# Performance work log

Measured on AMD Instinct MI355X. Metric: run time of the kernel, lower is better.

Reference implementation:

```python
import jax, jax.numpy as jnp
import numpy as np
import math

B, L, H, D, HID = 2, 1024, 16, 64, 1024  # batch, seq, heads, head_dim, hidden_size


def _rope_tables(seq_len, dim):
    inv_freq = 1.0 / (10000.0 ** (jnp.arange(0, dim, 2, dtype=jnp.float32) / dim))
    t = jnp.arange(seq_len, dtype=jnp.float32)
    freqs = jnp.outer(t, inv_freq)            # (L, D/2)
    emb = jnp.concatenate([freqs, freqs], -1)  # (L, D)
    return jnp.cos(emb), jnp.sin(emb)


def _rotate_half(x):
    x1, x2 = jnp.split(x, 2, axis=-1)
    return jnp.concatenate([-x2, x1], axis=-1)


def _apply_rope(x, cos, sin):
    # x: (B,H,L,D); cos/sin: (1,1,L,D)
    return x * cos + _rotate_half(x) * sin


def setup_inputs() -> dict:
    key = jax.random.key(0)
    ks = jax.random.split(key, 8)
    s = 0.02
    return {
        "x": jax.random.normal(ks[0], (B, L, HID), jnp.float32),
        "w_qkv": jax.random.normal(ks[1], (HID, 3 * H * D), jnp.float32) * s,
        "w_o": jax.random.normal(ks[2], (H * D, HID), jnp.float32) * s,
        "log_p": jax.random.normal(ks[3], (H, 1, 1), jnp.float32) * 0.02,
        "log_a": jax.random.normal(ks[4], (H, 1, 1), jnp.float32) * 0.02,
        "w1": jax.random.normal(ks[5], (2 * H, 2 * H), jnp.float32) * s,
        "b1": jnp.zeros((2 * H,), jnp.float32),
        "w2": jax.random.normal(ks[6], (2 * H, H), jnp.float32) * s,
        "b2": jnp.zeros((H,), jnp.float32),
    }


def _forward(x, w_qkv, w_o, log_p, log_a, w1, b1, w2, b2):
    Bx, Lx, _ = x.shape
    qkv = jnp.dot(x, w_qkv).reshape(Bx, Lx, 3, H, D)
    qkv = jnp.transpose(qkv, (2, 0, 3, 1, 4))  # (3,B,H,L,D)
    q, k, v = qkv[0], qkv[1], qkv[2]

    cos, sin = _rope_tables(Lx, D)
    cos, sin = cos[None, None], sin[None, None]
    q = _apply_rope(q, cos, sin)
    k = _apply_rope(k, cos, sin)

    scale = 1.0 / math.sqrt(D)
    scores = jnp.einsum('bhid,bhjd->bhij', q, k) * scale  # (B,H,L,L)

    # Kerple bias: -p * log1p(a * |m-n|), per head
    pos = jnp.arange(Lx, dtype=jnp.float32)
    dist = jnp.abs(pos[None, :] - pos[:, None])            # (L,L)
    p = jax.nn.softplus(log_p)
    a = jax.nn.softplus(log_a)
    kerple = -p * jnp.log1p(a * dist[None])                # (H,L,L)

    # DAPE MLP refinement over head channel
    attn_t = jnp.transpose(scores, (0, 2, 3, 1))           # (B,L,L,H)
    kerple_t = jnp.broadcast_to(jnp.transpose(kerple, (1, 2, 0))[None], attn_t.shape)
    combined = jnp.concatenate([attn_t, kerple_t], axis=-1)  # (B,L,L,2H)
    hdn = jax.nn.gelu(jnp.dot(combined, w1) + b1, approximate=False)
    refined = jnp.dot(hdn, w2) + b2                        # (B,L,L,H)
    refined = jnp.transpose(refined, (0, 3, 1, 2))         # (B,H,L,L)

    scores = scores + kerple[None] + refined

    causal = jnp.tril(jnp.ones((Lx, Lx), dtype=bool))
    scores = jnp.where(causal[None, None], scores, -jnp.inf)
    weights = jax.nn.softmax(scores, axis=-1)
    out = jnp.einsum('bhij,bhjd->bhid', weights, v)        # (B,H,L,D)
    out = jnp.transpose(out, (0, 2, 1, 3)).reshape(Bx, Lx, H * D)
    return jnp.dot(out, w_o)


def reference(x, w_qkv, w_o, log_p, log_a, w1, b1, w2, b2):
    return _forward(x, w_qkv, w_o, log_p, log_a, w1, b1, w2, b2)
```

## Files before the change

### kernel.cpp

```cpp
#include <hip/hip_runtime.h>
#include <math.h>

#define Bv 2
#define Lv 1024
#define Hv 16
#define Dv 64
#define HIDv 1024

typedef unsigned short u16;
typedef short bf16x8 __attribute__((ext_vector_type(8)));
typedef unsigned short u16x4 __attribute__((ext_vector_type(4)));
typedef float f32x4 __attribute__((ext_vector_type(4)));

__device__ __forceinline__ u16 f2b(float f) {
    union { float f; unsigned u; } v; v.f = f;
    return (u16)((v.u + 0x8000u) >> 16);
}
__device__ __forceinline__ float b2f(u16 h) {
    union { unsigned u; float f; } v; v.u = ((unsigned)h) << 16;
    return v.f;
}

__device__ __forceinline__ void gl2lds16(const u16* g, u16* l) {
    __builtin_amdgcn_global_load_lds(
        (const __attribute__((address_space(1))) unsigned int*)g,
        (__attribute__((address_space(3))) unsigned int*)l,
        16, 0, 0);
}

__device__ __forceinline__ float gelu_fast(float x) {
    float x2 = x * x;
    float inner = __builtin_fmaf(0.044715f * x2, x, x);
    float e = __expf(-1.5957691216057308f * inner);
    return x * __builtin_amdgcn_rcpf(1.0f + e);
}

__global__ __launch_bounds__(256) void qkv_rope(
    const u16* __restrict__ A, const u16* __restrict__ B,
    const float* __restrict__ ctab, const float* __restrict__ stab,
    u16* __restrict__ q, u16* __restrict__ k, u16* __restrict__ vT)
{
    __shared__ __align__(16) char pool[64 * 136 * 2];
    u16* As = (u16*)pool;
    u16* Bs = (u16*)(pool + 8192);
    u16* Ct = (u16*)pool;

    const int m0 = blockIdx.y * 64;
    const int n0 = blockIdx.x * 128;
    const int K = 1024;

    const int tid = threadIdx.x;
    const int lane = tid & 63;
    const int wave = tid >> 6;
    const int wm0 = (wave >> 1) * 32;
    const int wn0 = (wave & 1) * 64;
    const int fr = lane & 15;
    const int fq = lane >> 4;

    f32x4 acc[2][4];
    #pragma unroll
    for (int i = 0; i < 2; ++i)
        #pragma unroll
        for (int j = 0; j < 4; ++j) acc[i][j] = (f32x4){0.f, 0.f, 0.f, 0.f};

    for (int k0 = 0; k0 < K; k0 += 32) {
        {
            int r = tid >> 2, ch = tid & 3;
            gl2lds16(A + (long long)(m0 + r) * K + k0 + ch * 8, &As[tid * 8]);
        }
        #pragma unroll
        for (int it = 0; it < 2; ++it) {
            int cid = tid + it * 256;
            int r = cid >> 2, ch = cid & 3;
            gl2lds16(B + (long long)(n0 + r) * K + k0 + ch * 8, &Bs[cid * 8]);
        }
        __syncthreads();
        bf16x8 af[2], bfr[4];
        #pragma unroll
        for (int i = 0; i < 2; ++i)
            af[i] = *(const bf16x8*)&As[(wm0 + i * 16 + fr) * 32 + fq * 8];
        #pragma unroll
        for (int j = 0; j < 4; ++j)
            bfr[j] = *(const bf16x8*)&Bs[(wn0 + j * 16 + fr) * 32 + fq * 8];
        #pragma unroll
        for (int i = 0; i < 2; ++i)
            #pragma unroll
            for (int j = 0; j < 4; ++j)
                acc[i][j] = __builtin_amdgcn_mfma_f32_16x16x32_bf16(
                    af[i], bfr[j], acc[i][j], 0, 0, 0);
        __syncthreads();
    }

    const int b = m0 >> 10;

    if (n0 >= 2048) {
        #pragma unroll
        for (int i = 0; i < 2; ++i)
            #pragma unroll
            for (int j = 0; j < 4; ++j) {
                int vcol = (n0 - 2048) + wn0 + j * 16 + fr;
                int head = vcol >> 6, d = vcol & 63;
                int l = ((m0 + wm0 + i * 16 + fq * 4) & 1023);
                u16 o[4];
                #pragma unroll
                for (int r = 0; r < 4; ++r) o[r] = f2b(acc[i][j][r]);
                *(u16x4*)&vT[((long long)(b * 16 + head) * 64 + d) * 1024 + l] =
                    *(u16x4*)o;
            }
        return;
    }

    #pragma unroll
    for (int i = 0; i < 2; ++i)
        #pragma unroll
        for (int j = 0; j < 4; ++j)
            #pragma unroll
            for (int r = 0; r < 4; ++r)
                Ct[(wm0 + i * 16 + fq * 4 + r) * 136 + wn0 + j * 16 + fr] =
                    f2b(acc[i][j][r]);
    __syncthreads();

    u16* dst = (n0 >= 1024) ? k : q;
    const int nh = n0 & 1023;
    #pragma unroll
    for (int c = 0; c < 4; ++c) {
        int cid = tid + c * 256;
        int row = cid >> 4, kc = cid & 15;
        int l = (m0 + row) & 1023;
        int head = (nh >> 6) + (kc >> 3);
        int d0 = (kc & 7) * 8;
        bf16x8 x  = *(const bf16x8*)&Ct[row * 136 + kc * 8];
        bf16x8 xp = *(const bf16x8*)&Ct[row * 136 + (kc ^ 4) * 8];
        float4 c0 = *(const float4*)&ctab[l * 64 + d0];
        float4 c1 = *(const float4*)&ctab[l * 64 + d0 + 4];
        float4 s0 = *(const float4*)&stab[l * 64 + d0];
        float4 s1 = *(const float4*)&stab[l * 64 + d0 + 4];
        float ct[8] = {c0.x, c0.y, c0.z, c0.w, c1.x, c1.y, c1.z, c1.w};
        float st[8] = {s0.x, s0.y, s0.z, s0.w, s1.x, s1.y, s1.z, s1.w};
        u16 o[8];
        #pragma unroll
        for (int e = 0; e < 8; ++e)
            o[e] = f2b(b2f((u16)x[e]) * ct[e] + b2f((u16)xp[e]) * st[e]);
        *(bf16x8*)&dst[((long long)(b * 16 + head) * 1024 + l) * 64 + d0] =
            *(bf16x8*)o;
    }
}

template<int BM, int BN, int WM, int WN, bool CBF16>
__global__ __launch_bounds__(256) void gemm_bt(
    const u16* __restrict__ A, const u16* __restrict__ B, void* __restrict__ Cv,
    int M, int N, int K, float alpha)
{
    constexpr int NW = BN / WN;
    constexpr int MI = WM / 16;
    constexpr int NI = WN / 16;
    constexpr int LDB = BN + 8;
    constexpr int LDF = BN + 4;
    __shared__ u16 As[BM * 32];
    __shared__ u16 Bs[BN * 32];
    __shared__ u16 Ctb[CBF16 ? BM * LDB : 1];
    __shared__ float Ctf[CBF16 ? 1 : BM * LDF];

    const int m0 = blockIdx.y * BM;
    const int n0 = blockIdx.x * BN;

    const int tid = threadIdx.x;
    const int lane = tid & 63;
    const int wave = tid >> 6;
    const int wm0 = (wave / NW) * WM;
    const int wn0 = (wave % NW) * WN;
    const int fr = lane & 15;
    const int fq = lane >> 4;

    f32x4 acc[MI][NI];
    #pragma unroll
    for (int i = 0; i < MI; ++i)
        #pragma unroll
        for (int j = 0; j < NI; ++j) acc[i][j] = (f32x4){0.f, 0.f, 0.f, 0.f};

    for (int k0 = 0; k0 < K; k0 += 32) {
        #pragma unroll
        for (int it = 0; it < BM / 64; ++it) {
            int cid = tid + it * 256;
            int r = cid >> 2, ch = cid & 3;
            gl2lds16(A + (long long)(m0 + r) * K + k0 + ch * 8, &As[cid * 8]);
        }
        #pragma unroll
        for (int it = 0; it < BN / 64; ++it) {
            int cid = tid + it * 256;
            int r = cid >> 2, ch = cid & 3;
            gl2lds16(B + (long long)(n0 + r) * K + k0 + ch * 8, &Bs[cid * 8]);
        }
        __syncthreads();
        bf16x8 af[MI], bfr[NI];
        #pragma unroll
        for (int i = 0; i < MI; ++i)
            af[i] = *(const bf16x8*)&As[(wm0 + i * 16 + fr) * 32 + fq * 8];
        #pragma unroll
        for (int j = 0; j < NI; ++j)
            bfr[j] = *(const bf16x8*)&Bs[(wn0 + j * 16 + fr) * 32 + fq * 8];
        #pragma unroll
        for (int i = 0; i < MI; ++i)
            #pragma unroll
            for (int j = 0; j < NI; ++j)
                acc[i][j] = __builtin_amdgcn_mfma_f32_16x16x32_bf16(
                    af[i], bfr[j], acc[i][j], 0, 0, 0);
        __syncthreads();
    }

    #pragma unroll
    for (int i = 0; i < MI; ++i)
        #pragma unroll
        for (int j = 0; j < NI; ++j)
            #pragma unroll
            for (int r = 0; r < 4; ++r) {
                int row = wm0 + i * 16 + fq * 4 + r;
                int col = wn0 + j * 16 + fr;
                float v = acc[i][j][r] * alpha;
                if (CBF16) Ctb[row * LDB + col] = f2b(v);
                else       Ctf[row * LDF + col] = v;
            }
    __syncthreads();
    if (CBF16) {
        constexpr int CPR = BN / 8;
        #pragma unroll
        for (int c = 0; c < (BM * BN) / (8 * 256); ++c) {
            int cid = tid + c * 256;
            int row = cid / CPR, kc = cid % CPR;
            *(bf16x8*)((u16*)Cv + (long long)(m0 + row) * N + n0 + kc * 8) =
                *(const bf16x8*)&Ctb[row * LDB + kc * 8];
        }
    } else {
        constexpr int CPR = BN / 4;
        #pragma unroll
        for (int c = 0; c < (BM * BN) / (4 * 256); ++c) {
            int cid = tid + c * 256;
            int row = cid / CPR, kc = cid % CPR;
            *(float4*)((float*)Cv + (long long)(m0 + row) * N + n0 + kc * 4) =
                *(const float4*)&Ctf[row * LDF + kc * 4];
        }
    }
}

__global__ __launch_bounds__(256) void qk_direct(
    const u16* __restrict__ Q, const u16* __restrict__ K, u16* __restrict__ S)
{
    const int m0 = blockIdx.y * 128;
    const int n0 = blockIdx.x * 128;
    if (n0 > m0) return;
    const u16* A = Q + (long long)blockIdx.z * 65536;
    const u16* B = K + (long long)blockIdx.z * 65536;
    u16* C = S + (long long)blockIdx.z * 1048576;

    __shared__ u16 Ct[128 * 136];

    const int tid = threadIdx.x;
    const int lane = tid & 63;
    const int wave = tid >> 6;
    const int wm0 = (wave >> 1) * 64;
    const int wn0 = (wave & 1) * 64;
    const int fr = lane & 15;
    const int fq = lane >> 4;

    bf16x8 af[4][2], bfr[4][2];
    #pragma unroll
    for (int i = 0; i < 4; ++i)
        #pragma unroll
        for (int p = 0; p < 2; ++p) {
            af[i][p]  = *(const bf16x8*)&A[(m0 + wm0 + i * 16 + fr) * 64 + p * 32 + fq * 8];
            bfr[i][p] = *(const bf16x8*)&B[(n0 + wn0 + i * 16 + fr) * 64 + p * 32 + fq * 8];
        }

    f32x4 acc[4][4];
    #pragma unroll
    for (int i = 0; i < 4; ++i)
        #pragma unroll
        for (int j = 0; j < 4; ++j) acc[i][j] = (f32x4){0.f, 0.f, 0.f, 0.f};

    #pragma unroll
    for (int p = 0; p < 2; ++p)
        #pragma unroll
        for (int i = 0; i < 4; ++i)
            #pragma unroll
            for (int j = 0; j < 4; ++j)
                acc[i][j] = __builtin_amdgcn_mfma_f32_16x16x32_bf16(
                    af[i][p], bfr[j][p], acc[i][j], 0, 0, 0);

    #pragma unroll
    for (int i = 0; i < 4; ++i)
        #pragma unroll
        for (int j = 0; j < 4; ++j)
            #pragma unroll
            for (int r = 0; r < 4; ++r)
                Ct[(wm0 + i * 16 + fq * 4 + r) * 136 + wn0 + j * 16 + fr] =
                    f2b(acc[i][j][r] * 0.125f);
    __syncthreads();
    #pragma unroll
    for (int c = 0; c < 8; ++c) {
        int cid = tid + c * 256;
        int row = cid >> 4, kc = cid & 15;
        *(bf16x8*)&C[(long long)(m0 + row) * 1024 + n0 + kc * 8] =
            *(const bf16x8*)&Ct[row * 136 + kc * 8];
    }
}

__global__ __launch_bounds__(256) void pv_direct(
    const u16* __restrict__ W, const u16* __restrict__ VT, u16* __restrict__ O)
{
    const int m0 = blockIdx.x * 64;
    const int bh = blockIdx.y;
    const u16* A = W + (long long)bh * 1048576;
    const u16* B = VT + (long long)bh * 65536;
    const int b = bh >> 4, h = bh & 15;

    __shared__ u16 Ct[64 * 72];

    const int tid = threadIdx.x;
    const int lane = tid & 63;
    const int wave = tid >> 6;
    const int wm0 = (wave >> 1) * 32;
    const int wn0 = (wave & 1) * 32;
    const int fr = lane & 15;
    const int fq = lane >> 4;

    f32x4 acc[2][2];
    #pragma unroll
    for (int i = 0; i < 2; ++i)
        #pragma unroll
        for (int j = 0; j < 2; ++j) acc[i][j] = (f32x4){0.f, 0.f, 0.f, 0.f};

    const int Kend = m0 + 64;
    for (int k0 = 0; k0 < Kend; k0 += 64) {
        bf16x8 af[2][2], bfr[2][2];
        #pragma unroll
        for (int p = 0; p < 2; ++p) {
            #pragma unroll
            for (int i = 0; i < 2; ++i)
                af[p][i] = *(const bf16x8*)&A[(m0 + wm0 + i * 16 + fr) * 1024 + k0 + p * 32 + fq * 8];
            #pragma unroll
            for (int j = 0; j < 2; ++j)
                bfr[p][j] = *(const bf16x8*)&B[(wn0 + j * 16 + fr) * 1024 + k0 + p * 32 + fq * 8];
        }
        #pragma unroll
        for (int p = 0; p < 2; ++p)
            #pragma unroll
            for (int i = 0; i < 2; ++i)
                #pragma unroll
                for (int j = 0; j < 2; ++j)
                    acc[i][j] = __builtin_amdgcn_mfma_f32_16x16x32_bf16(
                        af[p][i], bfr[p][j], acc[i][j], 0, 0, 0);
    }

    #pragma unroll
    for (int i = 0; i < 2; ++i)
        #pragma unroll
        for (int j = 0; j < 2; ++j)
            #pragma unroll
            for (int r = 0; r < 4; ++r)
                Ct[(wm0 + i * 16 + fq * 4 + r) * 72 + wn0 + j * 16 + fr] =
                    f2b(acc[i][j][r]);
    __syncthreads();
    const long long ob = (long long)b * 1048576 + h * 64;
    #pragma unroll
    for (int c = 0; c < 2; ++c) {
        int cid = tid + c * 256;
        int row = cid >> 3, kc = cid & 7;
        *(bf16x8*)&O[ob + (long long)(m0 + row) * 1024 + kc * 8] =
            *(const bf16x8*)&Ct[row * 72 + kc * 8];
    }
}

__global__ __launch_bounds__(256) void prep(
    const float* __restrict__ x, u16* __restrict__ x_bf,
    const float* __restrict__ w_qkv, u16* __restrict__ wqkvT,
    const float* __restrict__ w_o, u16* __restrict__ woT,
    const float* __restrict__ log_p, const float* __restrict__ log_a,
    u16* __restrict__ ktab, float* __restrict__ ctab, float* __restrict__ stab)
{
    __shared__ float tile[64][65];
    const int bid = blockIdx.x;
    const int tid = threadIdx.x;

    if (bid < 8192) {
        int i = bid * 256 + tid;
        x_bf[i] = f2b(x[i]);
        return;
    }
    if (bid >= 9280) {
        int idx = (bid - 9280) * 256 + tid;
        int e = idx & 65535;
        int l = e >> 6, d = e & 63;
        float inv_freq = __expf((float)(d & 31) * -0.28782313662425574f);
        float arg = (float)l * inv_freq;
        if (idx < 65536) ctab[e] = __cosf(arg);
        else             stab[e] = (d < 32) ? -__sinf(arg) : __sinf(arg);
        return;
    }
    if (bid >= 9216) {
        int idx = (bid - 9216) * 256 + tid;
        int h = idx & 15, dist = idx >> 4;
        float pp = log1pf(__expf(log_p[h]));
        float aa = log1pf(__expf(log_a[h]));
        ktab[idx] = f2b(-pp * log1pf(aa * (float)dist));
        return;
    }
    const float* src; u16* dst; int M, N, bx, by;
    if (bid < 8960) { int t = bid - 8192; bx = t % 48; by = t / 48; src = w_qkv; dst = wqkvT; M = 1024; N = 3072; }
    else            { int t = bid - 8960; bx = t % 16; by = t / 16; src = w_o;   dst = woT;   M = 1024; N = 1024; }
    const int m0 = by * 64, n0 = bx * 64;
    #pragma unroll
    for (int c = 0; c < 4; ++c) {
        int f = tid + c * 256;
        int r = f >> 4, cs = (f & 15) * 4;
        float4 v = *(const float4*)&src[(long long)(m0 + r) * N + n0 + cs];
        tile[r][cs] = v.x; tile[r][cs + 1] = v.y;
        tile[r][cs + 2] = v.z; tile[r][cs + 3] = v.w;
    }
    __syncthreads();
    int nl = tid >> 2, ms = (tid & 3) * 16;
    u16 outv[16];
    #pragma unroll
    for (int c = 0; c < 16; ++c) outv[c] = f2b(tile[ms + c][nl]);
    *(bf16x8*)&dst[(long long)(n0 + nl) * M + m0 + ms]     = *(bf16x8*)&outv[0];
    *(bf16x8*)&dst[(long long)(n0 + nl) * M + m0 + ms + 8] = *(bf16x8*)&outv[8];
}

#define LSTR 1044

__global__ __launch_bounds__(512) void dape_soft(
    u16* __restrict__ S, const u16* __restrict__ ktab,
    const float* __restrict__ w1, const float* __restrict__ b1,
    const float* __restrict__ w2, const float* __restrict__ b2)
{
    const int i = 1023 - blockIdx.x;
    const int b = blockIdx.y;

    __shared__ u16 logits[16 * LSTR];
    __shared__ u16 comb[256 * 36];

    const int tid = threadIdx.x;
    const int lane = tid & 63;
    const int wave = tid >> 6;
    const int fr = lane & 15;
    const int fq = lane >> 4;

    bf16x8 B1a, B1b, B2f, Bid;
    #pragma unroll
    for (int e = 0; e < 8; ++e) {
        int c = fq * 8 + e;
        B1a[e] = (short)f2b(w1[c * 32 + fr]);
        B1b[e] = (short)f2b(w1[c * 32 + 16 + fr]);
        B2f[e] = (short)f2b(w2[c * 16 + fr]);
        Bid[e] = (short)((c == fr || c == 16 + fr) ? 0x3F80 : 0);
    }
    const float b1a = b1[fr], b1b = b1[16 + fr], b2v = b2[fr];

    const long long sbase = (long long)b * 16 * 1048576 + (long long)i * 1024;
    const int nchunk = (i >> 8) + 1;
    const int slast = i >> 8;

    for (int c = 0; c < nchunk; ++c) {
        {
            const int jo = tid & 255;
            const int half = tid >> 8;
            const int j = c * 256 + jo;
            u16 row[8];
            #pragma unroll
            for (int h = 0; h < 8; ++h)
                row[h] = S[sbase + (long long)(half * 8 + h) * 1048576 + j];
            const int dist = (i - j > 0) ? (i - j) : 0;
            *(bf16x8*)&comb[jo * 36 + half * 8] = *(bf16x8*)row;
            *(bf16x8*)&comb[jo * 36 + 16 + half * 8] =
                *(const bf16x8*)&ktab[dist * 16 + half * 8];
        }
        __syncthreads();

        for (int t = wave; t < 16; t += 8) {
            const int jt = c * 256 + t * 16;
            if (jt > i) continue;

            bf16x8 A1 = *(const bf16x8*)&comb[(t * 16 + fr) * 36 + fq * 8];
            f32x4 z = (f32x4){0.f, 0.f, 0.f, 0.f};
            f32x4 ac1a = __builtin_amdgcn_mfma_f32_16x16x32_bf16(A1, B1a, z, 0, 0, 0);
            f32x4 ac1b = __builtin_amdgcn_mfma_f32_16x16x32_bf16(A1, B1b, z, 0, 0, 0);
            f32x4 cres = __builtin_amdgcn_mfma_f32_16x16x32_bf16(
                A1, Bid, (f32x4){b2v, b2v, b2v, b2v}, 0, 0, 0);

            u16* hidp = &comb[t * 16 * 36];
            #pragma unroll
            for (int r = 0; r < 4; ++r) {
                float g0 = gelu_fast(ac1a[r] + b1a);
                float g1 = gelu_fast(ac1b[r] + b1b);
                hidp[(fq * 4 + r) * 36 + fr]      = f2b(g0);
                hidp[(fq * 4 + r) * 36 + 16 + fr] = f2b(g1);
            }
            bf16x8 A2 = *(const bf16x8*)&hidp[fr * 36 + fq * 8];
            f32x4 ac2 = __builtin_amdgcn_mfma_f32_16x16x32_bf16(A2, B2f, cres, 0, 0, 0);

            u16 o[4];
            #pragma unroll
            for (int r = 0; r < 4; ++r) o[r] = f2b(ac2[r]);
            *(u16x4*)&logits[fr * LSTR + jt + fq * 4] = *(u16x4*)o;
        }
        __syncthreads();
    }

    const int we = ((i >> 7) + 1) << 7;
    for (int hh = wave; hh < 16; hh += 8) {
        float vals[16];
        float mx = -3.0e38f;
        #pragma unroll
        for (int s = 0; s < 4; ++s) {
            if (s > slast) continue;
            u16x4 r4 = *(const u16x4*)&logits[hh * LSTR + lane * 4 + 256 * s];
            if (s < slast) {
                #pragma unroll
                for (int e = 0; e < 4; ++e) {
                    float v = b2f(r4[e]);
                    vals[s * 4 + e] = v;
                    mx = fmaxf(mx, v);
                }
            } else {
                #pragma unroll
                for (int e = 0; e < 4; ++e) {
                    int j = lane * 4 + 256 * s + e;
                    float v = (j <= i) ? b2f(r4[e]) : -3.0e38f;
                    vals[s * 4 + e] = v;
                    mx = fmaxf(mx, v);
                }
            }
        }
        #pragma unroll
        for (int off = 1; off < 64; off <<= 1)
            mx = fmaxf(mx, __shfl_xor(mx, off));
        float sm = 0.f;
        #pragma unroll
        for (int s = 0; s < 4; ++s) {
            if (s > slast) continue;
            if (s < slast) {
                #pragma unroll
                for (int e = 0; e < 4; ++e) {
                    float ev = __expf(vals[s * 4 + e] - mx);
                    vals[s * 4 + e] = ev;
                    sm += ev;
                }
            } else {
                #pragma unroll
                for (int e = 0; e < 4; ++e) {
                    float ev = (vals[s * 4 + e] > -1.0e37f)
                                   ? __expf(vals[s * 4 + e] - mx) : 0.f;
                    vals[s * 4 + e] = ev;
                    sm += ev;
                }
            }
        }
        #pragma unroll
        for (int off = 1; off < 64; off <<= 1)
            sm += __shfl_xor(sm, off);
        const float inv = __builtin_amdgcn_rcpf(sm);
        const long long hb = sbase + (long long)hh * 1048576;
        #pragma unroll
        for (int s = 0; s < 4; ++s) {
            if (s > slast) continue;
            int j0v = lane * 4 + 256 * s;
            if (s < slast) {
                u16 o[4];
                #pragma unroll
                for (int e = 0; e < 4; ++e) o[e] = f2b(vals[s * 4 + e] * inv);
                *(u16x4*)&S[hb + j0v] = *(u16x4*)o;
            } else if (j0v < we) {
                u16 o[4];
                #pragma unroll
                for (int e = 0; e < 4; ++e) o[e] = f2b(vals[s * 4 + e] * inv);
                *(u16x4*)&S[hb + j0v] = *(u16x4*)o;
            }
        }
    }
}

extern "C" void kernel_launch(void* const* d_in, const int* in_sizes, int n_in,
                              void* d_out, int out_size, void* d_ws, size_t ws_size,
                              hipStream_t stream)
{
    const float* x     = (const float*)d_in[0];
    const float* w_qkv = (const float*)d_in[1];
    const float* w_o   = (const float*)d_in[2];
    const float* log_p = (const float*)d_in[3];
    const float* log_a = (const float*)d_in[4];
    const float* w1    = (const float*)d_in[5];
    const float* b1    = (const float*)d_in[6];
    const float* w2    = (const float*)d_in[7];
    const float* b2    = (const float*)d_in[8];
    float* out = (float*)d_out;

    char* p = (char*)d_ws;
    u16* x_bf    = (u16*)p;    p += 2097152ll * 2;
    u16* wqkvT   = (u16*)p;    p += 3145728ll * 2;
    u16* woT     = (u16*)p;    p += 1048576ll * 2;
    u16* q_bf    = (u16*)p;    p += 2097152ll * 2;
    u16* k_bf    = (u16*)p;    p += 2097152ll * 2;
    u16* vT      = (u16*)p;    p += 2097152ll * 2;
    u16* scores  = (u16*)p;    p += 33554432ll * 2;
    u16* attn_bf = (u16*)p;    p += 2097152ll * 2;
    u16* ktab    = (u16*)p;    p += 16384ll * 2;
    float* ctab  = (float*)p;  p += 65536ll * 4;
    float* stab  = (float*)p;  p += 65536ll * 4;

    prep<<<9792, 256, 0, stream>>>(x, x_bf, w_qkv, wqkvT, w_o, woT,
                                   log_p, log_a, ktab, ctab, stab);

    qkv_rope<<<dim3(24, 32), 256, 0, stream>>>(
        x_bf, wqkvT, ctab, stab, q_bf, k_bf, vT);

    qk_direct<<<dim3(8, 8, 32), 256, 0, stream>>>(q_bf, k_bf, scores);

    dape_soft<<<dim3(1024, 2), 512, 0, stream>>>(
        scores, ktab, w1, b1, w2, b2);

    pv_direct<<<dim3(16, 32), 256, 0, stream>>>(scores, vT, attn_bf);

    gemm_bt<64, 64, 32, 32, false><<<dim3(16, 32, 1), 256, 0, stream>>>(
        attn_bf, woT, out, 2048, 1024, 1024, 1.0f);
}
```

Before: 215.1 us.

## Write QK scores in head-innermost layout and stream DAPE tiles directly from global

```diff
diff --git a/kernel.cpp b/kernel.cpp
--- a/kernel.cpp
+++ b/kernel.cpp
@@ -242,65 +242,66 @@
     }
 }
 
-__global__ __launch_bounds__(256) void qk_direct(
-    const u16* __restrict__ Q, const u16* __restrict__ K, u16* __restrict__ S)
+__global__ __launch_bounds__(256) void qk_allh(
+    const u16* __restrict__ Q, const u16* __restrict__ K, u16* __restrict__ St)
 {
-    const int m0 = blockIdx.y * 128;
-    const int n0 = blockIdx.x * 128;
-    if (n0 > m0) return;
-    const u16* A = Q + (long long)blockIdx.z * 65536;
-    const u16* B = K + (long long)blockIdx.z * 65536;
-    u16* C = S + (long long)blockIdx.z * 1048576;
-
-    __shared__ u16 Ct[128 * 136];
+    const int n0 = blockIdx.x * 64;
+    const int m0 = blockIdx.y * 32;
+    if (n0 > m0 + 31) return;
+    const int b = blockIdx.z;
 
     const int tid = threadIdx.x;
     const int lane = tid & 63;
     const int wave = tid >> 6;
-    const int wm0 = (wave >> 1) * 64;
-    const int wn0 = (wave & 1) * 64;
     const int fr = lane & 15;
     const int fq = lane >> 4;
 
-    bf16x8 af[4][2], bfr[4][2];
-    #pragma unroll
-    for (int i = 0; i < 4; ++i)
+    const long long qkbase = (long long)b * 16 * 65536;
+    u16* Sb = St + (long long)b * 1024 * 1024 * 16;
+
+    for (int hh = 0; hh < 4; ++hh) {
+        const int h = wave * 4 + hh;
+        const u16* A  = Q + qkbase + (long long)h * 65536;
+        const u16* Bp = K + qkbase + (long long)h * 65536;
+
+        bf16x8 af[2][2], bf[4][2];
         #pragma unroll
         for (int p = 0; p < 2; ++p) {
-            af[i][p]  = *(const bf16x8*)&A[(m0 + wm0 + i * 16 + fr) * 64 + p * 32 + fq * 8];
-            bfr[i][p] = *(const bf16x8*)&B[(n0 + wn0 + i * 16 + fr) * 64 + p * 32 + fq * 8];
-        }
-
-    f32x4 acc[4][4];
-    #pragma unroll
-    for (int i = 0; i < 4; ++i)
-        #pragma unroll
-        for (int j = 0; j < 4; ++j) acc[i][j] = (f32x4){0.f, 0.f, 0.f, 0.f};
-
-    #pragma unroll
-    for (int p = 0; p < 2; ++p)
-        #pragma unroll
-        for (int i = 0; i < 4; ++i)
+            #pragma unroll
+            for (int ii = 0; ii < 2; ++ii)
+                af[ii][p] = *(const bf16x8*)&A[(m0 + ii * 16 + fr) * 64 + p * 32 + fq * 8];
             #pragma unroll
             for (int j = 0; j < 4; ++j)
-                acc[i][j] = __builtin_amdgcn_mfma_f32_16x16x32_bf16(
-                    af[i][p], bfr[j][p], acc[i][j], 0, 0, 0);
-
-    #pragma unroll
-    for (int i = 0; i < 4; ++i)
-        #pragma unroll
-        for (int j = 0; j < 4; ++j)
-            #pragma unroll
-            for (int r = 0; r < 4; ++r)
-                Ct[(wm0 + i * 16 + fq * 4 + r) * 136 + wn0 + j * 16 + fr] =
-                    f2b(acc[i][j][r] * 0.125f);
-    __syncthreads();
-    #pragma unroll
-    for (int c = 0; c < 8; ++c) {
-        int cid = tid + c * 256;
-        int row = cid >> 4, kc = cid & 15;
-        *(bf16x8*)&C[(long long)(m0 + row) * 1024 + n0 + kc * 8] =
-            *(const bf16x8*)&Ct[row * 136 + kc * 8];
+                bf[j][p]  = *(const bf16x8*)&Bp[(n0 + j * 16 + fr) * 64 + p * 32 + fq * 8];
+        }
+
+        f32x4 acc[2][4];
+        #pragma unroll
+        for (int ii = 0; ii < 2; ++ii)
+            #pragma unroll
+            for (int j = 0; j < 4; ++j) acc[ii][j] = (f32x4){0.f, 0.f, 0.f, 0.f};
+
+        #pragma unroll
+        for (int p = 0; p < 2; ++p)
+            #pragma unroll
+            for (int ii = 0; ii < 2; ++ii)
+                #pragma unroll
+                for (int j = 0; j < 4; ++j)
+                    acc[ii][j] = __builtin_amdgcn_mfma_f32_16x16x32_bf16(
+                        af[ii][p], bf[j][p], acc[ii][j], 0, 0, 0);
+
+        #pragma unroll
+        for (int ii = 0; ii < 2; ++ii)
+            #pragma unroll
+            for (int j = 0; j < 4; ++j) {
+                const int jj = n0 + j * 16 + fr;
+                #pragma unroll
+                for (int r = 0; r < 4; ++r) {
+                    const int irow = m0 + ii * 16 + fq * 4 + r;
+                    Sb[((long long)irow * 1024 + jj) * 16 + h] =
+                        f2b(acc[ii][j][r] * 0.125f);
+                }
+            }
     }
 }
 
@@ -428,7 +429,8 @@
 #define LSTR 1044
 
 __global__ __launch_bounds__(512) void dape_soft(
-    u16* __restrict__ S, const u16* __restrict__ ktab,
+    const u16* __restrict__ St, u16* __restrict__ W,
+    const u16* __restrict__ ktab,
     const float* __restrict__ w1, const float* __restrict__ b1,
     const float* __restrict__ w2, const float* __restrict__ b2)
 {
@@ -436,7 +438,7 @@
     const int b = blockIdx.y;
 
     __shared__ u16 logits[16 * LSTR];
-    __shared__ u16 comb[256 * 36];
+    __shared__ u16 hid[8][16 * 36];
 
     const int tid = threadIdx.x;
     const int lane = tid & 63;
@@ -455,56 +457,56 @@
     }
     const float b1a = b1[fr], b1b = b1[16 + fr], b2v = b2[fr];
 
+    const long long sti = ((long long)b * 1024 + i) * 1024;
+    const int ntile = (i >> 4) + 1;
+    const int slast = i >> 8;
+    u16* hidp = &hid[wave][0];
+
+    bf16x8 cur;
+    {
+        int t0 = (wave < ntile) ? wave : 0;
+        int j = t0 * 16 + fr;
+        int dist = i - j; if (dist < 0) dist = 0;
+        const u16* pp = (fq < 2) ? &St[(sti + j) * 16 + fq * 8]
+                                 : &ktab[dist * 16 + (fq - 2) * 8];
+        cur = *(const bf16x8*)pp;
+    }
+    for (int t = wave; t < ntile; t += 8) {
+        bf16x8 nxt = cur;
+        if (t + 8 < ntile) {
+            int j = (t + 8) * 16 + fr;
+            int dist = i - j; if (dist < 0) dist = 0;
+            const u16* pp = (fq < 2) ? &St[(sti + j) * 16 + fq * 8]
+                                     : &ktab[dist * 16 + (fq - 2) * 8];
+            nxt = *(const bf16x8*)pp;
+        }
+
+        f32x4 z = (f32x4){0.f, 0.f, 0.f, 0.f};
+        f32x4 ac1a = __builtin_amdgcn_mfma_f32_16x16x32_bf16(cur, B1a, z, 0, 0, 0);
+        f32x4 ac1b = __builtin_amdgcn_mfma_f32_16x16x32_bf16(cur, B1b, z, 0, 0, 0);
+        f32x4 cres = __builtin_amdgcn_mfma_f32_16x16x32_bf16(
+            cur, Bid, (f32x4){b2v, b2v, b2v, b2v}, 0, 0, 0);
+
+        #pragma unroll
+        for (int r = 0; r < 4; ++r) {
+            float g0 = gelu_fast(ac1a[r] + b1a);
+            float g1 = gelu_fast(ac1b[r] + b1b);
+            hidp[(fq * 4 + r) * 36 + fr]      = f2b(g0);
+            hidp[(fq * 4 + r) * 36 + 16 + fr] = f2b(g1);
+        }
+        bf16x8 A2 = *(const bf16x8*)&hidp[fr * 36 + fq * 8];
+        f32x4 ac2 = __builtin_amdgcn_mfma_f32_16x16x32_bf16(A2, B2f, cres, 0, 0, 0);
+
+        u16 o[4];
+        #pragma unroll
+        for (int r = 0; r < 4; ++r) o[r] = f2b(ac2[r]);
+        *(u16x4*)&logits[fr * LSTR + t * 16 + fq * 4] = *(u16x4*)o;
+
+        cur = nxt;
+    }
+    __syncthreads();
+
     const long long sbase = (long long)b * 16 * 1048576 + (long long)i * 1024;
-    const int nchunk = (i >> 8) + 1;
-    const int slast = i >> 8;
-
-    for (int c = 0; c < nchunk; ++c) {
-        {
-            const int jo = tid & 255;
-            const int half = tid >> 8;
-            const int j = c * 256 + jo;
-            u16 row[8];
-            #pragma unroll
-            for (int h = 0; h < 8; ++h)
-                row[h] = S[sbase + (long long)(half * 8 + h) * 1048576 + j];
-            const int dist = (i - j > 0) ? (i - j) : 0;
-            *(bf16x8*)&comb[jo * 36 + half * 8] = *(bf16x8*)row;
-            *(bf16x8*)&comb[jo * 36 + 16 + half * 8] =
-                *(const bf16x8*)&ktab[dist * 16 + half * 8];
-        }
-        __syncthreads();
-
-        for (int t = wave; t < 16; t += 8) {
-            const int jt = c * 256 + t * 16;
-            if (jt > i) continue;
-
-            bf16x8 A1 = *(const bf16x8*)&comb[(t * 16 + fr) * 36 + fq * 8];
-            f32x4 z = (f32x4){0.f, 0.f, 0.f, 0.f};
-            f32x4 ac1a = __builtin_amdgcn_mfma_f32_16x16x32_bf16(A1, B1a, z, 0, 0, 0);
-            f32x4 ac1b = __builtin_amdgcn_mfma_f32_16x16x32_bf16(A1, B1b, z, 0, 0, 0);
-            f32x4 cres = __builtin_amdgcn_mfma_f32_16x16x32_bf16(
-                A1, Bid, (f32x4){b2v, b2v, b2v, b2v}, 0, 0, 0);
-
-            u16* hidp = &comb[t * 16 * 36];
-            #pragma unroll
-            for (int r = 0; r < 4; ++r) {
-                float g0 = gelu_fast(ac1a[r] + b1a);
-                float g1 = gelu_fast(ac1b[r] + b1b);
-                hidp[(fq * 4 + r) * 36 + fr]      = f2b(g0);
-                hidp[(fq * 4 + r) * 36 + 16 + fr] = f2b(g1);
-            }
-            bf16x8 A2 = *(const bf16x8*)&hidp[fr * 36 + fq * 8];
-            f32x4 ac2 = __builtin_amdgcn_mfma_f32_16x16x32_bf16(A2, B2f, cres, 0, 0, 0);
-
-            u16 o[4];
-            #pragma unroll
-            for (int r = 0; r < 4; ++r) o[r] = f2b(ac2[r]);
-            *(u16x4*)&logits[fr * LSTR + jt + fq * 4] = *(u16x4*)o;
-        }
-        __syncthreads();
-    }
-
     const int we = ((i >> 7) + 1) << 7;
     for (int hh = wave; hh < 16; hh += 8) {
         float vals[16];
@@ -567,12 +569,12 @@
                 u16 o[4];
                 #pragma unroll
                 for (int e = 0; e < 4; ++e) o[e] = f2b(vals[s * 4 + e] * inv);
-                *(u16x4*)&S[hb + j0v] = *(u16x4*)o;
+                *(u16x4*)&W[hb + j0v] = *(u16x4*)o;
             } else if (j0v < we) {
                 u16 o[4];
                 #pragma unroll
                 for (int e = 0; e < 4; ++e) o[e] = f2b(vals[s * 4 + e] * inv);
-                *(u16x4*)&S[hb + j0v] = *(u16x4*)o;
+                *(u16x4*)&W[hb + j0v] = *(u16x4*)o;
             }
         }
     }
@@ -600,7 +602,8 @@
     u16* q_bf    = (u16*)p;    p += 2097152ll * 2;
     u16* k_bf    = (u16*)p;    p += 2097152ll * 2;
     u16* vT      = (u16*)p;    p += 2097152ll * 2;
-    u16* scores  = (u16*)p;    p += 33554432ll * 2;
+    u16* scoresW = (u16*)p;    p += 33554432ll * 2;
+    u16* St      = (u16*)p;    p += 33554432ll * 2;
     u16* attn_bf = (u16*)p;    p += 2097152ll * 2;
     u16* ktab    = (u16*)p;    p += 16384ll * 2;
     float* ctab  = (float*)p;  p += 65536ll * 4;
@@ -612,12 +615,12 @@
     qkv_rope<<<dim3(24, 32), 256, 0, stream>>>(
         x_bf, wqkvT, ctab, stab, q_bf, k_bf, vT);
 
-    qk_direct<<<dim3(8, 8, 32), 256, 0, stream>>>(q_bf, k_bf, scores);
+    qk_allh<<<dim3(16, 32, 2), 256, 0, stream>>>(q_bf, k_bf, St);
 
     dape_soft<<<dim3(1024, 2), 512, 0, stream>>>(
-        scores, ktab, w1, b1, w2, b2);
-
-    pv_direct<<<dim3(16, 32), 256, 0, stream>>>(scores, vT, attn_bf);
+        St, scoresW, ktab, w1, b1, w2, b2);
+
+    pv_direct<<<dim3(16, 32), 256, 0, stream>>>(scoresW, vT, attn_bf);
 
     gemm_bt<64, 64, 32, 32, false><<<dim3(16, 32, 1), 256, 0, stream>>>(
         attn_bf, woT, out, 2048, 1024, 1024, 1.0f);
```

Measured after the change: 255.0 us. 18.5% more time.
